# Kernel optimization log

Hardware: AMD Instinct MI355X
Metric: run time of the kernel (lower is better)

The kernel has to match this reference:

```python
import jax, jax.numpy as jnp
import numpy as np

D_MODEL = 512
H = 8
D_K = D_MODEL // H


def setup_inputs() -> dict:
    key = jax.random.key(0)
    ks = jax.random.split(key, 11)
    B, S = 2, 2048
    scale = 1.0 / np.sqrt(D_MODEL)
    return {
        "q": jax.random.normal(ks[0], (B, S, D_MODEL), jnp.float32),
        "v": jax.random.normal(ks[1], (B, S, D_MODEL), jnp.float32),
        "k": jax.random.normal(ks[2], (B, S, D_MODEL), jnp.float32),
        "w_q": jax.random.normal(ks[3], (D_MODEL, D_MODEL), jnp.float32) * scale,
        "b_q": jnp.zeros((D_MODEL,), jnp.float32),
        "w_k": jax.random.normal(ks[4], (D_MODEL, D_MODEL), jnp.float32) * scale,
        "b_k": jnp.zeros((D_MODEL,), jnp.float32),
        "w_v": jax.random.normal(ks[5], (D_MODEL, D_MODEL), jnp.float32) * scale,
        "b_v": jnp.zeros((D_MODEL,), jnp.float32),
        "w_o": jax.random.normal(ks[6], (D_MODEL, D_MODEL), jnp.float32) * scale,
        "b_o": jnp.zeros((D_MODEL,), jnp.float32),
    }


def reference(q, v, k, w_q, b_q, w_k, b_k, w_v, b_v, w_o, b_o):
    B, S, _ = q.shape
    # projections (nn.Linear: x @ W.T + b)
    query = q @ w_q.T + b_q
    key_t = k @ w_k.T + b_k
    value = v @ w_v.T + b_v
    # split heads: [B, S, H, D_K] -> [B, H, S, D_K]
    query = query.reshape(B, S, H, D_K).transpose(0, 2, 1, 3)
    key_t = key_t.reshape(B, S, H, D_K).transpose(0, 2, 1, 3)
    value = value.reshape(B, S, H, D_K).transpose(0, 2, 1, 3)
    # unfused attention: full [B, H, S, S] score matrix
    scores = jnp.einsum("bhqd,bhkd->bhqk", query, key_t) / jnp.sqrt(
        jnp.asarray(D_K, query.dtype)
    )
    attn = jax.nn.softmax(scores, axis=-1)  # dropout inactive in eval
    x = jnp.einsum("bhqk,bhkd->bhqd", attn, value)
    # merge heads and output projection
    x = x.transpose(0, 2, 1, 3).reshape(B, S, D_MODEL)
    return x @ w_o.T + b_o
```

## Files before the change

### kernel.cpp

```cpp
#include <hip/hip_runtime.h>
#include <hip/hip_bf16.h>


typedef __attribute__((ext_vector_type(8))) short short8;
typedef __attribute__((ext_vector_type(4))) short short4v;
typedef __attribute__((ext_vector_type(4))) float f32x4;
typedef __attribute__((ext_vector_type(2))) unsigned int uint2v;

#define DM 512
#define SEQ 2048
#define NROW 4096
#define LOG2E 1.44269504088896341f
#define MFMA(a, b, c) __builtin_amdgcn_mfma_f32_16x16x32_bf16(a, b, c, 0, 0, 0)
#define FENCE() __asm__ __volatile__("" ::: "memory")

#if __has_builtin(__builtin_amdgcn_exp2f)
#define EXP2(x) __builtin_amdgcn_exp2f(x)
#else
#define EXP2(x) exp2f(x)
#endif

__device__ __forceinline__ float bf_bits2f(short s) {
    unsigned int u = ((unsigned int)(unsigned short)s) << 16;
    return __builtin_bit_cast(float, u);
}
__device__ __forceinline__ short f2bf_r(float f) {
    unsigned int u = __builtin_bit_cast(unsigned int, f) + 0x8000u;
    return (short)(u >> 16);
}
__device__ __forceinline__ unsigned int pack_bf16(float lo, float hi) {
    unsigned int ul = __builtin_bit_cast(unsigned int, lo) + 0x8000u;
    unsigned int uh = __builtin_bit_cast(unsigned int, hi) + 0x8000u;
    return __builtin_amdgcn_perm(uh, ul, 0x07060302u);
}

__device__ __forceinline__ void gload_lds16(const void* src, void* lds_dst) {
    __builtin_amdgcn_global_load_lds(
        (const __attribute__((address_space(1))) unsigned int*)src,
        (__attribute__((address_space(3))) unsigned int*)lds_dst, 16, 0, 0);
}

template <int ROWS, int NW>
__device__ __forceinline__ void stage_tile(const short* __restrict__ gsrc, size_t gstride,
                                           short* lds, int wave, int lane) {
    constexpr int ISSUES = ROWS * 8 / (64 * NW);
    #pragma unroll
    for (int i = 0; i < ISSUES; i++) {
        const int blk = i * NW + wave;
        const int g = blk * 64 + lane;
        const int row = g >> 3;
        const int cb = (g & 7) ^ (row & 7);
        gload_lds16(gsrc + (size_t)row * gstride + cb * 8, lds + (size_t)blk * 512);
    }
}

__device__ __forceinline__ bool detect_f32(const unsigned int* __restrict__ q, int* cnt_lds) {
    if (threadIdx.x == 0) *cnt_lds = 0;
    __syncthreads();
    int local = 0;
    for (int i = threadIdx.x; i < 1024; i += blockDim.x) {
        unsigned int lo = q[i] & 0x7FFFu;
        if (lo >= 0x3000u && lo < 0x4400u) local++;
    }
    if (local) atomicAdd(cnt_lds, local);
    __syncthreads();
    return *cnt_lds < 512;
}

struct ConvArgs { const void* src[11]; short* dst[11]; int n[11]; };
__global__ void convert_all(ConvArgs a) {
    __shared__ int cnt;
    const bool f32m = detect_f32((const unsigned int*)a.src[0], &cnt);
    const int tid = blockIdx.x * 256 + threadIdx.x;
    const int stride = gridDim.x * 256;
    if (f32m) {
        for (int s = 0; s < 11; s++) {
            const float4* sp = (const float4*)a.src[s];
            short4v* dp = (short4v*)a.dst[s];
            const int n4 = a.n[s] >> 2;
            for (int i = tid; i < n4; i += stride) {
                float4 v = sp[i];
                short4v o;
                o[0] = f2bf_r(v.x); o[1] = f2bf_r(v.y);
                o[2] = f2bf_r(v.z); o[3] = f2bf_r(v.w);
                dp[i] = o;
            }
        }
    } else {
        for (int s = 0; s < 11; s++) {
            const short4v* sp = (const short4v*)a.src[s];
            short4v* dp = (short4v*)a.dst[s];
            const int n4 = a.n[s] >> 2;
            for (int i = tid; i < n4; i += stride) dp[i] = sp[i];
        }
    }
}

template <int MT>
__device__ __forceinline__ void gemm_core(const short* __restrict__ A,
                                          const short* __restrict__ W,
                                          int m0, int n0, short* Alds, short* Blds,
                                          int wave, int lane, f32x4 (&acc)[MT / 64][4]) {
    const int rc = lane & 15, quad = lane >> 4;
    const short* Ag = A + (size_t)m0 * DM;
    const short* Bg = W + (size_t)n0 * DM;
    constexpr int ABUF = MT * 64, BBUF = 64 * 64;
    constexpr int INFLIGHT = MT * 8 / 256 + 2;
    constexpr int NITER = DM / 64;

    stage_tile<MT, 4>(Ag, DM, Alds, wave, lane);
    stage_tile<64, 4>(Bg, DM, Blds, wave, lane);

    for (int i = 0; i < NITER; i++) {
        const int cur = i & 1;
        const short* Ac = Alds + cur * ABUF;
        const short* Bc = Blds + cur * BBUF;
        if (i + 1 < NITER) {
            stage_tile<MT, 4>(Ag + (i + 1) * 64, DM, Alds + (cur ^ 1) * ABUF, wave, lane);
            stage_tile<64, 4>(Bg + (i + 1) * 64, DM, Blds + (cur ^ 1) * BBUF, wave, lane);
            __builtin_amdgcn_s_waitcnt(0x3F70 | INFLIGHT);
        } else {
            __builtin_amdgcn_s_waitcnt(0x3F70);
        }
        FENCE();
        __builtin_amdgcn_s_barrier();
        FENCE();
        #pragma unroll
        for (int h = 0; h < 2; h++) {
            short8 bf[4];
            #pragma unroll
            for (int nt = 0; nt < 4; nt++) {
                const int br = nt * 16 + rc;
                bf[nt] = *(const short8*)&Bc[br * 64 + (((quad + 4 * h) ^ (br & 7)) * 8)];
            }
            #pragma unroll
            for (int ms = 0; ms < MT / 64; ms++) {
                const int ar = wave * (MT / 4) + ms * 16 + rc;
                short8 af = *(const short8*)&Ac[ar * 64 + (((quad + 4 * h) ^ (ar & 7)) * 8)];
                #pragma unroll
                for (int nt = 0; nt < 4; nt++)
                    acc[ms][nt] = MFMA(af, bf[nt], acc[ms][nt]);
            }
        }
        FENCE();
        __builtin_amdgcn_s_barrier();
        FENCE();
    }
}

struct QKVArgs {
    const short* A[3]; const short* W[3]; const short* Bi[3];
    short* Cq; short* Ck; short* Cv;
};
__global__ __launch_bounds__(256, 3) void qkv_gemm(QKVArgs args) {
    __shared__ __align__(16) short Alds[2][128 * 64];
    __shared__ __align__(16) short Blds[2][64 * 64];
    const int z = blockIdx.z;
    const int wave = threadIdx.x >> 6, lane = threadIdx.x & 63;
    const int rc = lane & 15, quad = lane >> 4;
    const int m0 = blockIdx.x * 128, n0 = blockIdx.y * 64;

    f32x4 acc[2][4] = {};
    gemm_core<128>(args.A[z], args.W[z], m0, n0, &Alds[0][0], &Blds[0][0], wave, lane, acc);
    const short* bias = args.Bi[z];

    if (z == 2) {
        const int hh = n0 >> 6;
        #pragma unroll
        for (int ms = 0; ms < 2; ms++) {
            const int mw = m0 + wave * 32 + ms * 16;
            const int b = mw >> 11, sb = (mw & 2047) + quad * 4;
            #pragma unroll
            for (int nt = 0; nt < 4; nt++) {
                const int d = nt * 16 + rc;
                const float bv = bf_bits2f(bias[n0 + d]);
                short4v pk;
                #pragma unroll
                for (int r = 0; r < 4; r++) pk[r] = f2bf_r(acc[ms][nt][r] + bv);
                *(short4v*)(args.Cv + ((size_t)((b * 8 + hh) * 64 + d)) * SEQ + sb) = pk;
            }
        }
    } else {
        short* C = (z == 0) ? args.Cq : args.Ck;
        const float sc = (z == 0) ? (0.125f * LOG2E) : 1.0f;
        #pragma unroll
        for (int ms = 0; ms < 2; ms++) {
            const int mw = m0 + wave * 32 + ms * 16;
            #pragma unroll
            for (int nt = 0; nt < 4; nt++) {
                const int col = n0 + nt * 16 + rc;
                const float bv = bf_bits2f(bias[col]);
                #pragma unroll
                for (int r = 0; r < 4; r++)
                    C[(size_t)(mw + quad * 4 + r) * DM + col] = f2bf_r((acc[ms][nt][r] + bv) * sc);
            }
        }
    }
}

__global__ __launch_bounds__(256, 4) void out_gemm(
    const short* __restrict__ A, const short* __restrict__ W,
    const short* __restrict__ bias, void* __restrict__ Cout,
    const unsigned int* __restrict__ qraw) {
    __shared__ __align__(16) short Alds[2][64 * 64];
    __shared__ __align__(16) short Blds[2][64 * 64];
    __shared__ int cnt;
    const bool f32out = detect_f32(qraw, &cnt);
    const int wave = threadIdx.x >> 6, lane = threadIdx.x & 63;
    const int rc = lane & 15, quad = lane >> 4;
    const int m0 = blockIdx.x * 64, n0 = blockIdx.y * 64;
    f32x4 acc[1][4] = {};
    gemm_core<64>(A, W, m0, n0, &Alds[0][0], &Blds[0][0], wave, lane, acc);
    const int mw = m0 + wave * 16;
    #pragma unroll
    for (int nt = 0; nt < 4; nt++) {
        const int col = n0 + nt * 16 + rc;
        const float bv = bf_bits2f(bias[col]);
        #pragma unroll
        for (int r = 0; r < 4; r++) {
            const size_t idx = (size_t)(mw + quad * 4 + r) * DM + col;
            const float val = acc[0][nt][r] + bv;
            if (f32out) ((float*)Cout)[idx] = val;
            else        ((short*)Cout)[idx] = f2bf_r(val);
        }
    }
}

__global__ __launch_bounds__(256, 2) void attn_kernel(
    const short* __restrict__ Q, const short* __restrict__ K,
    const short* __restrict__ Vt, float* __restrict__ Opart,
    float* __restrict__ Lpart)
{
    __shared__ __align__(16) short Klds[2][64 * 64];
    __shared__ __align__(16) short Vlds[2][64 * 64];
    __shared__ __align__(16) short Plds[4][32 * 72];

    const int wave = threadIdx.x >> 6, lane = threadIdx.x & 63;
    const int rc = lane & 15, quad = lane >> 4;
    const int bh = blockIdx.y, z = blockIdx.z;
    const size_t baseQ = (size_t)(bh >> 3) * SEQ * DM + (size_t)(bh & 7) * 64;
    const short* Qb = Q + baseQ;
    const short* Kb = K + baseQ + (size_t)(z * 1024) * DM;
    const short* Vb = Vt + (size_t)bh * 64 * SEQ + z * 1024;
    const int q0 = blockIdx.x * 128 + wave * 32;

    short8 qa[2][2];
    #pragma unroll
    for (int ms = 0; ms < 2; ms++)
        #pragma unroll
        for (int h = 0; h < 2; h++)
            qa[ms][h] = *(const short8*)(Qb + (size_t)(q0 + ms * 16 + rc) * DM + h * 32 + quad * 8);

    short8 ones;
    #pragma unroll
    for (int j = 0; j < 8; j++) ones[j] = (short)0x3F80;

    f32x4 o[2][4] = {};
    f32x4 lsum[2] = {};
    short* Pw = &Plds[wave][0];

    int koff[4][2], voff[4][2];
    #pragma unroll
    for (int kt = 0; kt < 4; kt++) {
        const int row = rc * 4 + kt;
        #pragma unroll
        for (int h = 0; h < 2; h++)
            koff[kt][h] = row * 64 + (((quad + 4 * h) ^ (row & 7)) * 8);
    }
    #pragma unroll
    for (int dt = 0; dt < 4; dt++) {
        const int row = dt * 16 + rc;
        #pragma unroll
        for (int h = 0; h < 2; h++)
            voff[dt][h] = row * 64 + (((quad + 4 * h) ^ (row & 7)) * 8);
    }

    stage_tile<64, 4>(Kb, DM, &Klds[0][0], wave, lane);
    stage_tile<64, 4>(Vb, SEQ, &Vlds[0][0], wave, lane);

    auto body = [&](int it, int cur) {
        if (it + 1 < 16) {
            const int k0n = (it + 1) * 64;
            stage_tile<64, 4>(Kb + (size_t)k0n * DM, DM, &Klds[cur ^ 1][0], wave, lane);
            stage_tile<64, 4>(Vb + k0n, SEQ, &Vlds[cur ^ 1][0], wave, lane);
            __builtin_amdgcn_s_waitcnt(0x3F74);
        } else {
            __builtin_amdgcn_s_waitcnt(0x3F70);
        }
        FENCE();
        __builtin_amdgcn_s_barrier();
        FENCE();

        const short* Kt = &Klds[cur][0];
        const short* Vl = &Vlds[cur][0];

        short8 kf[4][2];
        #pragma unroll
        for (int kt = 0; kt < 4; kt++)
            #pragma unroll
            for (int h = 0; h < 2; h++)
                kf[kt][h] = *(const short8*)&Kt[koff[kt][h]];
        f32x4 s[2][4];
        #pragma unroll
        for (int ms = 0; ms < 2; ms++)
            #pragma unroll
            for (int kt = 0; kt < 4; kt++) {
                f32x4 t = {};
                t = MFMA(qa[ms][0], kf[kt][0], t);
                t = MFMA(qa[ms][1], kf[kt][1], t);
                s[ms][kt] = t;
            }
        #pragma unroll
        for (int ms = 0; ms < 2; ms++)
            #pragma unroll
            for (int r = 0; r < 4; r++) {
                uint2v pk;
                pk[0] = pack_bf16(EXP2(s[ms][0][r]), EXP2(s[ms][1][r]));
                pk[1] = pack_bf16(EXP2(s[ms][2][r]), EXP2(s[ms][3][r]));
                *(uint2v*)(&Pw[(ms * 16 + quad * 4 + r) * 72 + rc * 4]) = pk;
            }
        __builtin_amdgcn_s_waitcnt(0xC07F);
        short8 pa[2][2];
        #pragma unroll
        for (int ms = 0; ms < 2; ms++)
            #pragma unroll
            for (int h = 0; h < 2; h++)
                pa[ms][h] = *(const short8*)(&Pw[(ms * 16 + rc) * 72 + h * 32 + quad * 8]);
        #pragma unroll
        for (int ms = 0; ms < 2; ms++) {
            lsum[ms] = MFMA(pa[ms][0], ones, lsum[ms]);
            lsum[ms] = MFMA(pa[ms][1], ones, lsum[ms]);
        }
        #pragma unroll
        for (int dt = 0; dt < 4; dt++) {
            short8 v0 = *(const short8*)&Vl[voff[dt][0]];
            short8 v1 = *(const short8*)&Vl[voff[dt][1]];
            #pragma unroll
            for (int ms = 0; ms < 2; ms++) {
                o[ms][dt] = MFMA(pa[ms][0], v0, o[ms][dt]);
                o[ms][dt] = MFMA(pa[ms][1], v1, o[ms][dt]);
            }
        }
        FENCE();
        __builtin_amdgcn_s_barrier();
        FENCE();
    };

    for (int itp = 0; itp < 16; itp += 2) {
        body(itp, 0);
        body(itp + 1, 1);
    }

    const size_t obase = ((size_t)(z * 16 + bh)) * SEQ;
    #pragma unroll
    for (int ms = 0; ms < 2; ms++) {
        const int qrow = q0 + ms * 16 + quad * 4;
        if (rc == 0) {
            #pragma unroll
            for (int r = 0; r < 4; r++)
                Lpart[obase + qrow + r] = lsum[ms][r];
        }
        #pragma unroll
        for (int dt = 0; dt < 4; dt++)
            #pragma unroll
            for (int r = 0; r < 4; r++)
                Opart[(obase + qrow + r) * 64 + dt * 16 + rc] = o[ms][dt][r];
    }
}

__global__ void attn_reduce(const float* __restrict__ Opart, const float* __restrict__ Lpart,
                            short* __restrict__ X) {
    const int idx = blockIdx.x * 256 + threadIdx.x;
    const int dq = idx & 15;
    const int bhq = idx >> 4;
    const int bh = bhq >> 11, q = bhq & 2047;
    const float4 o0 = ((const float4*)Opart)[(size_t)bhq * 16 + dq];
    const float4 o1 = ((const float4*)Opart)[(size_t)(bhq + 16 * SEQ) * 16 + dq];
    const float inv = 1.0f / (Lpart[bhq] + Lpart[bhq + 16 * SEQ]);
    short4v pk;
    pk[0] = f2bf_r((o0.x + o1.x) * inv);
    pk[1] = f2bf_r((o0.y + o1.y) * inv);
    pk[2] = f2bf_r((o0.z + o1.z) * inv);
    pk[3] = f2bf_r((o0.w + o1.w) * inv);
    const size_t row = (size_t)(bh >> 3) * SEQ + q;
    *(short4v*)(&X[row * DM + (bh & 7) * 64 + dq * 4]) = pk;
}

extern "C" void kernel_launch(void* const* d_in, const int* in_sizes, int n_in,
                              void* d_out, int out_size, void* d_ws, size_t ws_size,
                              hipStream_t stream) {
    char* ws = (char*)d_ws;
    const size_t SEQB = (size_t)NROW * DM * sizeof(short);
    const size_t WB   = (size_t)DM * DM * sizeof(short);
    const size_t BB   = (size_t)DM * sizeof(short);

    size_t off = 0;
    short* qc = (short*)(ws + off); off += SEQB;
    short* vc = (short*)(ws + off); off += SEQB;
    short* kc = (short*)(ws + off); off += SEQB;
    short* wq = (short*)(ws + off); off += WB;
    short* wk = (short*)(ws + off); off += WB;
    short* wv = (short*)(ws + off); off += WB;
    short* wo = (short*)(ws + off); off += WB;
    short* bq = (short*)(ws + off); off += BB;
    short* bk = (short*)(ws + off); off += BB;
    short* bv = (short*)(ws + off); off += BB;
    short* bo = (short*)(ws + off); off += BB;
    off = (off + 255) & ~(size_t)255;
    short* Qp  = (short*)(ws + off); off += SEQB;
    short* Kp  = (short*)(ws + off); off += SEQB;
    short* Vtp = (short*)(ws + off); off += SEQB;
    short* Xp  = (short*)(ws + off); off += SEQB;
    float* Opart = (float*)(ws + off); off += (size_t)2 * 16 * SEQ * 64 * sizeof(float);
    float* Lpart = (float*)(ws + off); off += (size_t)2 * 16 * SEQ * sizeof(float);

    ConvArgs ca;
    const void* srcs[11] = {d_in[0], d_in[1], d_in[2], d_in[3], d_in[5], d_in[7],
                            d_in[9], d_in[4], d_in[6], d_in[8], d_in[10]};
    short* dsts[11] = {qc, vc, kc, wq, wk, wv, wo, bq, bk, bv, bo};
    int ns[11] = {NROW * DM, NROW * DM, NROW * DM, DM * DM, DM * DM, DM * DM,
                  DM * DM, DM, DM, DM, DM};
    for (int i = 0; i < 11; i++) { ca.src[i] = srcs[i]; ca.dst[i] = dsts[i]; ca.n[i] = ns[i]; }
    convert_all<<<1024, 256, 0, stream>>>(ca);

    QKVArgs qa;
    qa.A[0] = qc; qa.A[1] = kc; qa.A[2] = vc;
    qa.W[0] = wq; qa.W[1] = wk; qa.W[2] = wv;
    qa.Bi[0] = bq; qa.Bi[1] = bk; qa.Bi[2] = bv;
    qa.Cq = Qp; qa.Ck = Kp; qa.Cv = Vtp;
    qkv_gemm<<<dim3(NROW / 128, DM / 64, 3), 256, 0, stream>>>(qa);

    attn_kernel<<<dim3(SEQ / 128, 16, 2), 256, 0, stream>>>(Qp, Kp, Vtp, Opart, Lpart);
    attn_reduce<<<dim3(16 * SEQ * 16 / 256), 256, 0, stream>>>(Opart, Lpart, Xp);

    out_gemm<<<dim3(NROW / 64, DM / 64), 256, 0, stream>>>(
        Xp, wo, bo, d_out, (const unsigned int*)d_in[0]);
}
```

Measured before the change: 151.7 us.

## Drop split-K attention and reduce kernel; process full key range per block

The attention kernel no longer splits the key sequence into two halves with partial outputs and a separate reduction kernel. Each block now covers 64 query rows (16 per wave) over all 2048 keys, normalises in-register and writes bf16 X directly. MFMA operands are swapped so each lane holds one query row's output, block indices are remapped across heads, and s_setprio is raised around the MFMA sections. This removes the fp32 partial-output round trip and one launch, but halves per-wave query reuse of K/V tiles and doubles the loop length per block.

New measurement: 156.1 us. 1.03x slower.

```diff
diff --git a/kernel.cpp b/kernel.cpp
--- a/kernel.cpp
+++ b/kernel.cpp
@@ -228,35 +228,34 @@
 
 __global__ __launch_bounds__(256, 2) void attn_kernel(
     const short* __restrict__ Q, const short* __restrict__ K,
-    const short* __restrict__ Vt, float* __restrict__ Opart,
-    float* __restrict__ Lpart)
+    const short* __restrict__ Vt, short* __restrict__ X)
 {
     __shared__ __align__(16) short Klds[2][64 * 64];
     __shared__ __align__(16) short Vlds[2][64 * 64];
-    __shared__ __align__(16) short Plds[4][32 * 72];
+    __shared__ __align__(16) short Plds[4][16 * 72];
 
     const int wave = threadIdx.x >> 6, lane = threadIdx.x & 63;
     const int rc = lane & 15, quad = lane >> 4;
-    const int bh = blockIdx.y, z = blockIdx.z;
-    const size_t baseQ = (size_t)(bh >> 3) * SEQ * DM + (size_t)(bh & 7) * 64;
-    const short* Qb = Q + baseQ;
-    const short* Kb = K + baseQ + (size_t)(z * 1024) * DM;
-    const short* Vb = Vt + (size_t)bh * 64 * SEQ + z * 1024;
-    const int q0 = blockIdx.x * 128 + wave * 32;
-
-    short8 qa[2][2];
-    #pragma unroll
-    for (int ms = 0; ms < 2; ms++)
-        #pragma unroll
-        for (int h = 0; h < 2; h++)
-            qa[ms][h] = *(const short8*)(Qb + (size_t)(q0 + ms * 16 + rc) * DM + h * 32 + quad * 8);
+    const int L = blockIdx.x;
+    const int bh = (L & 7) * 2 + ((L >> 3) >> 5);
+    const int qb = (L >> 3) & 31;
+    const size_t baseQK = (size_t)(bh >> 3) * SEQ * DM + (size_t)(bh & 7) * 64;
+    const short* Qb = Q + baseQK;
+    const short* Kb = K + baseQK;
+    const short* Vb = Vt + (size_t)bh * 64 * SEQ;
+    const int q0 = qb * 64 + wave * 16;
+
+    short8 qa[2];
+    #pragma unroll
+    for (int h = 0; h < 2; h++)
+        qa[h] = *(const short8*)(Qb + (size_t)(q0 + rc) * DM + h * 32 + quad * 8);
 
     short8 ones;
     #pragma unroll
     for (int j = 0; j < 8; j++) ones[j] = (short)0x3F80;
 
-    f32x4 o[2][4] = {};
-    f32x4 lsum[2] = {};
+    f32x4 o[4] = {};
+    f32x4 lsum = {};
     short* Pw = &Plds[wave][0];
 
     int koff[4][2], voff[4][2];
@@ -279,7 +278,7 @@
     stage_tile<64, 4>(Vb, SEQ, &Vlds[0][0], wave, lane);
 
     auto body = [&](int it, int cur) {
-        if (it + 1 < 16) {
+        if (it + 1 < 32) {
             const int k0n = (it + 1) * 64;
             stage_tile<64, 4>(Kb + (size_t)k0n * DM, DM, &Klds[cur ^ 1][0], wave, lane);
             stage_tile<64, 4>(Vb + k0n, SEQ, &Vlds[cur ^ 1][0], wave, lane);
@@ -300,90 +299,59 @@
             #pragma unroll
             for (int h = 0; h < 2; h++)
                 kf[kt][h] = *(const short8*)&Kt[koff[kt][h]];
-        f32x4 s[2][4];
-        #pragma unroll
-        for (int ms = 0; ms < 2; ms++)
-            #pragma unroll
-            for (int kt = 0; kt < 4; kt++) {
-                f32x4 t = {};
-                t = MFMA(qa[ms][0], kf[kt][0], t);
-                t = MFMA(qa[ms][1], kf[kt][1], t);
-                s[ms][kt] = t;
-            }
-        #pragma unroll
-        for (int ms = 0; ms < 2; ms++)
-            #pragma unroll
-            for (int r = 0; r < 4; r++) {
-                uint2v pk;
-                pk[0] = pack_bf16(EXP2(s[ms][0][r]), EXP2(s[ms][1][r]));
-                pk[1] = pack_bf16(EXP2(s[ms][2][r]), EXP2(s[ms][3][r]));
-                *(uint2v*)(&Pw[(ms * 16 + quad * 4 + r) * 72 + rc * 4]) = pk;
-            }
+        f32x4 s[4];
+        __builtin_amdgcn_s_setprio(1);
+        #pragma unroll
+        for (int kt = 0; kt < 4; kt++) {
+            f32x4 t = {};
+            t = MFMA(qa[0], kf[kt][0], t);
+            t = MFMA(qa[1], kf[kt][1], t);
+            s[kt] = t;
+        }
+        __builtin_amdgcn_s_setprio(0);
+        #pragma unroll
+        for (int r = 0; r < 4; r++) {
+            uint2v pk;
+            pk[0] = pack_bf16(EXP2(s[0][r]), EXP2(s[1][r]));
+            pk[1] = pack_bf16(EXP2(s[2][r]), EXP2(s[3][r]));
+            *(uint2v*)(&Pw[(quad * 4 + r) * 72 + rc * 4]) = pk;
+        }
         __builtin_amdgcn_s_waitcnt(0xC07F);
-        short8 pa[2][2];
-        #pragma unroll
-        for (int ms = 0; ms < 2; ms++)
-            #pragma unroll
-            for (int h = 0; h < 2; h++)
-                pa[ms][h] = *(const short8*)(&Pw[(ms * 16 + rc) * 72 + h * 32 + quad * 8]);
-        #pragma unroll
-        for (int ms = 0; ms < 2; ms++) {
-            lsum[ms] = MFMA(pa[ms][0], ones, lsum[ms]);
-            lsum[ms] = MFMA(pa[ms][1], ones, lsum[ms]);
-        }
+        short8 pa[2];
+        #pragma unroll
+        for (int h = 0; h < 2; h++)
+            pa[h] = *(const short8*)(&Pw[rc * 72 + h * 32 + quad * 8]);
+        __builtin_amdgcn_s_setprio(1);
+        lsum = MFMA(ones, pa[0], lsum);
+        lsum = MFMA(ones, pa[1], lsum);
         #pragma unroll
         for (int dt = 0; dt < 4; dt++) {
             short8 v0 = *(const short8*)&Vl[voff[dt][0]];
             short8 v1 = *(const short8*)&Vl[voff[dt][1]];
-            #pragma unroll
-            for (int ms = 0; ms < 2; ms++) {
-                o[ms][dt] = MFMA(pa[ms][0], v0, o[ms][dt]);
-                o[ms][dt] = MFMA(pa[ms][1], v1, o[ms][dt]);
-            }
-        }
+            o[dt] = MFMA(v0, pa[0], o[dt]);
+            o[dt] = MFMA(v1, pa[1], o[dt]);
+        }
+        __builtin_amdgcn_s_setprio(0);
         FENCE();
         __builtin_amdgcn_s_barrier();
         FENCE();
     };
 
-    for (int itp = 0; itp < 16; itp += 2) {
+    for (int itp = 0; itp < 32; itp += 2) {
         body(itp, 0);
         body(itp + 1, 1);
     }
 
-    const size_t obase = ((size_t)(z * 16 + bh)) * SEQ;
-    #pragma unroll
-    for (int ms = 0; ms < 2; ms++) {
-        const int qrow = q0 + ms * 16 + quad * 4;
-        if (rc == 0) {
-            #pragma unroll
-            for (int r = 0; r < 4; r++)
-                Lpart[obase + qrow + r] = lsum[ms][r];
-        }
-        #pragma unroll
-        for (int dt = 0; dt < 4; dt++)
-            #pragma unroll
-            for (int r = 0; r < 4; r++)
-                Opart[(obase + qrow + r) * 64 + dt * 16 + rc] = o[ms][dt][r];
-    }
-}
-
-__global__ void attn_reduce(const float* __restrict__ Opart, const float* __restrict__ Lpart,
-                            short* __restrict__ X) {
-    const int idx = blockIdx.x * 256 + threadIdx.x;
-    const int dq = idx & 15;
-    const int bhq = idx >> 4;
-    const int bh = bhq >> 11, q = bhq & 2047;
-    const float4 o0 = ((const float4*)Opart)[(size_t)bhq * 16 + dq];
-    const float4 o1 = ((const float4*)Opart)[(size_t)(bhq + 16 * SEQ) * 16 + dq];
-    const float inv = 1.0f / (Lpart[bhq] + Lpart[bhq + 16 * SEQ]);
-    short4v pk;
-    pk[0] = f2bf_r((o0.x + o1.x) * inv);
-    pk[1] = f2bf_r((o0.y + o1.y) * inv);
-    pk[2] = f2bf_r((o0.z + o1.z) * inv);
-    pk[3] = f2bf_r((o0.w + o1.w) * inv);
-    const size_t row = (size_t)(bh >> 3) * SEQ + q;
-    *(short4v*)(&X[row * DM + (bh & 7) * 64 + dq * 4]) = pk;
+    const float inv = 1.0f / lsum[0];
+    short* Xr = X + baseQK;
+    const size_t rowoff = (size_t)(q0 + rc) * DM;
+    #pragma unroll
+    for (int dt = 0; dt < 4; dt++) {
+        short4v pk;
+        #pragma unroll
+        for (int r = 0; r < 4; r++) pk[r] = f2bf_r(o[dt][r] * inv);
+        *(short4v*)(Xr + rowoff + dt * 16 + quad * 4) = pk;
+    }
 }
 
 extern "C" void kernel_launch(void* const* d_in, const int* in_sizes, int n_in,
@@ -411,8 +379,6 @@
     short* Kp  = (short*)(ws + off); off += SEQB;
     short* Vtp = (short*)(ws + off); off += SEQB;
     short* Xp  = (short*)(ws + off); off += SEQB;
-    float* Opart = (float*)(ws + off); off += (size_t)2 * 16 * SEQ * 64 * sizeof(float);
-    float* Lpart = (float*)(ws + off); off += (size_t)2 * 16 * SEQ * sizeof(float);
 
     ConvArgs ca;
     const void* srcs[11] = {d_in[0], d_in[1], d_in[2], d_in[3], d_in[5], d_in[7],
@@ -430,8 +396,7 @@
     qa.Cq = Qp; qa.Ck = Kp; qa.Cv = Vtp;
     qkv_gemm<<<dim3(NROW / 128, DM / 64, 3), 256, 0, stream>>>(qa);
 
-    attn_kernel<<<dim3(SEQ / 128, 16, 2), 256, 0, stream>>>(Qp, Kp, Vtp, Opart, Lpart);
-    attn_reduce<<<dim3(16 * SEQ * 16 / 256), 256, 0, stream>>>(Opart, Lpart, Xp);
+    attn_kernel<<<dim3(512), 256, 0, stream>>>(Qp, Kp, Vtp, Xp);
 
     out_gemm<<<dim3(NROW / 64, DM / 64), 256, 0, stream>>>(
         Xp, wo, bo, d_out, (const unsigned int*)d_in[0]);
```
